# Kernel tuning notes

Hardware: AMD Instinct MI355X
Metric: run time of the kernel (lower is better)

Reference implementation:

```python
import jax, jax.numpy as jnp
import numpy as np
from jax import lax

HID = 256
BATCH = 256
INPUT_LEN = 512
N_SAMPLES = 16
HORIZON = 64


def _lstm_cell(x, h, c, Wih, Whh, b):
    # x: [B, in], h/c: [B, H]; PyTorch gate order i, f, g, o; b = b_ih + b_hh
    gates = x @ Wih.T + h @ Whh.T + b  # [B, 4H]
    i, f, g, o = jnp.split(gates, 4, axis=-1)
    c_new = jax.nn.sigmoid(f) * c + jax.nn.sigmoid(i) * jnp.tanh(g)
    h_new = jax.nn.sigmoid(o) * jnp.tanh(c_new)
    return h_new, c_new


def setup_inputs() -> dict:
    key = jax.random.key(0)
    ks = jax.random.split(key, 20)
    s = 1.0 / np.sqrt(HID)  # PyTorch LSTM init scale
    def u(k, shape):
        return jax.random.uniform(k, shape, jnp.float32, -s, s)
    inp = {
        "x": jax.random.normal(ks[0], (BATCH, INPUT_LEN), jnp.float32),
        "enc_Wih0": u(ks[1], (4 * HID, 1)),
        "enc_Whh0": u(ks[2], (4 * HID, HID)),
        "enc_b0": u(ks[3], (4 * HID,)),
        "enc_Wih1": u(ks[4], (4 * HID, HID)),
        "enc_Whh1": u(ks[5], (4 * HID, HID)),
        "enc_b1": u(ks[6], (4 * HID,)),
        "dec_Wih0": u(ks[7], (4 * HID, 1)),
        "dec_Whh0": u(ks[8], (4 * HID, HID)),
        "dec_b0": u(ks[9], (4 * HID,)),
        "dec_Wih1": u(ks[10], (4 * HID, HID)),
        "dec_Whh1": u(ks[11], (4 * HID, HID)),
        "dec_b1": u(ks[12], (4 * HID,)),
        "out_W": u(ks[13], (1, HID)),
        "out_b": u(ks[14], (1,)),
        # torch.rand(batch,1,1) per sample -> stacked over n_samples
        "dec_init": jax.random.uniform(ks[15], (N_SAMPLES, BATCH, 1), jnp.float32),
        "horizon": HORIZON,
    }
    return inp


def reference(x, enc_Wih0, enc_Whh0, enc_b0, enc_Wih1, enc_Whh1, enc_b1,
              dec_Wih0, dec_Whh0, dec_b0, dec_Wih1, dec_Whh1, dec_b1,
              out_W, out_b, dec_init, horizon):
    B, T = x.shape
    S = dec_init.shape[0]
    H = enc_Whh0.shape[1]

    # ---- encoder: 2-layer LSTM over input sequence ----
    xs = x.T[:, :, None]  # [T, B, 1]
    zero = jnp.zeros((B, H), x.dtype)

    def enc_step(carry, xt):
        h0, c0, h1, c1 = carry
        h0, c0 = _lstm_cell(xt, h0, c0, enc_Wih0, enc_Whh0, enc_b0)
        h1, c1 = _lstm_cell(h0, h1, c1, enc_Wih1, enc_Whh1, enc_b1)
        return (h0, c0, h1, c1), None

    (h0, c0, h1, c1), _ = lax.scan(enc_step, (zero, zero, zero, zero), xs)

    # ---- decoder: batch the independent n_samples together ----
    def rep(t):  # [B,H] -> [S*B,H]
        return jnp.broadcast_to(t, (S, B, H)).reshape(S * B, H)

    inp0 = dec_init.reshape(S * B, 1)

    def dec_step(carry, _):
        inp, h0, c0, h1, c1 = carry
        h0, c0 = _lstm_cell(inp, h0, c0, dec_Wih0, dec_Whh0, dec_b0)
        h1, c1 = _lstm_cell(h0, h1, c1, dec_Wih1, dec_Whh1, dec_b1)
        pred = h1 @ out_W.T + out_b  # [S*B, 1]
        return (pred, h0, c0, h1, c1), pred

    carry0 = (inp0, rep(h0), rep(c0), rep(h1), rep(c1))
    _, preds = lax.scan(dec_step, carry0, None, length=horizon)
    # preds: [T, S*B, 1] -> [B, S, T]
    return preds[:, :, 0].reshape(horizon, S, B).transpose(2, 1, 0)
```

## Files before the change

### kernel.cpp

```cpp
#include <hip/hip_runtime.h>
#include <stdint.h>


typedef short short8v __attribute__((ext_vector_type(8)));
typedef float float4v __attribute__((ext_vector_type(4)));
typedef unsigned long long u64;
#define MFMA(a,b,c) __builtin_amdgcn_mfma_f32_16x16x32_bf16((a),(b),(c),0,0,0)

#define HIDN 256
#define TLEN 512
#define HPE  ((size_t)256 * HIDN)
#define HPD  ((size_t)4096 * HIDN)

__device__ __forceinline__ unsigned short f2b(float f) {
    unsigned int u = __float_as_uint(f);
    unsigned int r = ((u >> 16) & 1u) + 0x7FFFu;
    return (unsigned short)((u + r) >> 16);
}
__device__ __forceinline__ float sigf(float x) { return 1.0f / (1.0f + __expf(-x)); }
__device__ __forceinline__ float tanhf2(float x) { return 1.0f - 2.0f / (1.0f + __expf(2.0f * x)); }

__device__ __forceinline__ void hpair_store(unsigned short* buf, int row, int hid,
                                            float h, int lane) {
    unsigned int mine = f2b(h);
    unsigned int part = (unsigned int)__shfl_xor((int)mine, 1);
    if (!(lane & 1)) {
        __hip_atomic_store((unsigned int*)&buf[(size_t)row * HIDN + hid],
                           mine | (part << 16),
                           __ATOMIC_RELAXED, __HIP_MEMORY_SCOPE_AGENT);
    }
}

__device__ __forceinline__ short8v ldA16(const unsigned short* p) {
    union { u64 d[2]; short8v v; } w;
    w.d[0] = __hip_atomic_load((const u64*)p,     __ATOMIC_RELAXED, __HIP_MEMORY_SCOPE_AGENT);
    w.d[1] = __hip_atomic_load((const u64*)p + 1, __ATOMIC_RELAXED, __HIP_MEMORY_SCOPE_AGENT);
    return w.v;
}

__device__ __forceinline__ void bar_sync(unsigned int* fl, int slot, unsigned int target,
                                         int nfl, int lane, int tid, int& dead) {
    __syncthreads();
    if (tid == 0)
        __hip_atomic_store(&fl[slot], target, __ATOMIC_RELAXED, __HIP_MEMORY_SCOPE_AGENT);
    if (tid < 64 && !dead) {
        int guard = 0;
        for (;;) {
            unsigned int v = 0xFFFFFFFFu;
            if (lane < nfl)
                v = __hip_atomic_load(&fl[lane], __ATOMIC_RELAXED, __HIP_MEMORY_SCOPE_AGENT);
            if (__ballot(v >= target) == ~0ull) break;
            if (++guard > (1 << 20)) { dead = 1; break; }
        }
    }
    __syncthreads();
    __builtin_amdgcn_fence(__ATOMIC_ACQUIRE, "workgroup");
}

__global__ __launch_bounds__(256) void pack_kernel(
    const float* __restrict__ Whh0, const float* __restrict__ Wih1,
    const float* __restrict__ Whh1, unsigned short* __restrict__ pk)
{
    int gid = blockIdx.x * 256 + threadIdx.x;
    int lane = gid & 63;
    int kc = (gid >> 6) & 7;
    int n  = (gid >> 9) & 63;
    int mat = gid >> 15;
    const float* W = (mat == 0) ? Whh0 : ((mat == 1) ? Wih1 : Whh1);
    const float* p = W + (size_t)(n * 16 + (lane & 15)) * HIDN
                       + (kc << 5) + ((lane >> 4) << 3);
    short8v v;
#pragma unroll
    for (int i = 0; i < 8; ++i) v[i] = (short)f2b(p[i]);
    *(short8v*)&pk[(size_t)gid << 3] = v;
}

__global__ __launch_bounds__(256, 1) void enc_kernel(
    const float* __restrict__ x,
    const float* __restrict__ Wih0, const float* __restrict__ Whh0, const float* __restrict__ b0,
    const float* __restrict__ Wih1, const float* __restrict__ Whh1, const float* __restrict__ b1,
    unsigned short* __restrict__ h0e, unsigned short* __restrict__ h1e,
    unsigned short* __restrict__ finh0, unsigned short* __restrict__ finh1,
    float* __restrict__ finc0, float* __restrict__ finc1,
    unsigned int* __restrict__ flags)
{
    const int tid = threadIdx.x, lane = tid & 63, wv = tid >> 6;
    const int bt = blockIdx.x & 15, hs = blockIdx.x >> 4;
    const int row0 = bt << 4, hidb = hs << 4;
    const int l15 = lane & 15, q = lane >> 4, q8 = q << 3;

    __shared__ float gt[12][16][17];
    __shared__ float xt[16][TLEN + 1];
    __shared__ unsigned short hst0[16][264], hst1[16][264];

    for (int idx = tid; idx < 16 * TLEN; idx += 256) {
        int r = idx >> 9, c = idx & 511;
        xt[r][c] = x[(size_t)(row0 + r) * TLEN + c];
    }

    short8v wf[3][8];
    {
        const float* Ws[3] = {Whh0, Wih1, Whh1};
#pragma unroll
        for (int j = 0; j < 3; ++j) {
            int p = wv * 3 + j;
            int mat = p >> 2, g = p & 3;
            const float* rp = Ws[mat] + (size_t)((g << 8) + hidb + l15) * HIDN + q8;
#pragma unroll
            for (int kc = 0; kc < 8; ++kc) {
                short8v v;
#pragma unroll
                for (int i = 0; i < 8; ++i) v[i] = (short)f2b(rp[(kc << 5) + i]);
                wf[j][kc] = v;
            }
        }
    }

    const int erow = tid >> 4, ehid = tid & 15;
    const int grow = row0 + erow, ghid = hidb + ehid;
    float wx[4], bb0v[4], bb1v[4];
#pragma unroll
    for (int g = 0; g < 4; ++g) {
        wx[g]   = Wih0[(g << 8) + ghid];
        bb0v[g] = b0[(g << 8) + ghid];
        bb1v[g] = b1[(g << 8) + ghid];
    }
    float c0 = 0.f, c1 = 0.f;
    unsigned int* fl = flags + (bt << 4);
    int dead = 0;
    const bool useH0 = (wv <= 2), useH1 = (wv >= 2);
    __syncthreads();

    for (int s = 1; s <= 513; ++s) {
        const unsigned short* hr0 = h0e + (size_t)((s - 1) & 1) * HPE;
        const unsigned short* hr1 = h1e + (size_t)((s - 1) & 1) * HPE;
        unsigned short* hw0 = h0e + (size_t)(s & 1) * HPE;
        unsigned short* hw1 = h1e + (size_t)(s & 1) * HPE;

        if (s >= 2) {
#pragma unroll
            for (int k = 0; k < 4; ++k) {
                int oo = tid + (k << 8);
                int r = oo >> 6, cu = oo & 63;
                u64 v = __hip_atomic_load((const u64*)&hr0[(size_t)(row0 + r) * HIDN + (cu << 2)],
                                          __ATOMIC_RELAXED, __HIP_MEMORY_SCOPE_AGENT);
                *(u64*)&hst0[r][cu << 2] = v;
            }
        }
        if (s >= 3) {
#pragma unroll
            for (int k = 0; k < 4; ++k) {
                int oo = tid + (k << 8);
                int r = oo >> 6, cu = oo & 63;
                u64 v = __hip_atomic_load((const u64*)&hr1[(size_t)(row0 + r) * HIDN + (cu << 2)],
                                          __ATOMIC_RELAXED, __HIP_MEMORY_SCOPE_AGENT);
                *(u64*)&hst1[r][cu << 2] = v;
            }
        }
        __syncthreads();

        float4v acc[3] = {{0,0,0,0},{0,0,0,0},{0,0,0,0}};
        short8v a0f[8], a1f[8];
        if (useH0 && s >= 2) {
#pragma unroll
            for (int kc = 0; kc < 8; ++kc) a0f[kc] = *(const short8v*)&hst0[l15][(kc << 5) + q8];
        }
        if (useH1 && s >= 3) {
#pragma unroll
            for (int kc = 0; kc < 8; ++kc) a1f[kc] = *(const short8v*)&hst1[l15][(kc << 5) + q8];
        }
#pragma unroll
        for (int j = 0; j < 3; ++j) {
            int p = wv * 3 + j;
            int mat = p >> 2;
            bool active = (mat == 0) ? (s >= 2 && s <= 512)
                        : (mat == 1) ? (s >= 2)
                                     : (s >= 3);
            if (active) {
                if (mat == 2) {
#pragma unroll
                    for (int kc = 0; kc < 8; ++kc) acc[j] = MFMA(a1f[kc], wf[j][kc], acc[j]);
                } else {
#pragma unroll
                    for (int kc = 0; kc < 8; ++kc) acc[j] = MFMA(a0f[kc], wf[j][kc], acc[j]);
                }
            }
        }
#pragma unroll
        for (int j = 0; j < 3; ++j) {
            int p = wv * 3 + j;
#pragma unroll
            for (int r = 0; r < 4; ++r) gt[p][(q << 2) + r][l15] = acc[j][r];
        }
        __syncthreads();

        if (s <= 512) {
            float xv = xt[erow][s - 1];
            float gi = gt[0][erow][ehid] + wx[0] * xv + bb0v[0];
            float gf = gt[1][erow][ehid] + wx[1] * xv + bb0v[1];
            float gg = gt[2][erow][ehid] + wx[2] * xv + bb0v[2];
            float go = gt[3][erow][ehid] + wx[3] * xv + bb0v[3];
            c0 = sigf(gf) * c0 + sigf(gi) * tanhf2(gg);
            float h0n = sigf(go) * tanhf2(c0);
            hpair_store(hw0, grow, ghid, h0n, lane);
            if (s == 512) {
                finh0[(size_t)grow * HIDN + ghid] = f2b(h0n);
                finc0[(size_t)grow * HIDN + ghid] = c0;
            }
        }
        if (s >= 2) {
            float gi = gt[4][erow][ehid] + gt[8][erow][ehid]  + bb1v[0];
            float gf = gt[5][erow][ehid] + gt[9][erow][ehid]  + bb1v[1];
            float gg = gt[6][erow][ehid] + gt[10][erow][ehid] + bb1v[2];
            float go = gt[7][erow][ehid] + gt[11][erow][ehid] + bb1v[3];
            c1 = sigf(gf) * c1 + sigf(gi) * tanhf2(gg);
            float h1n = sigf(go) * tanhf2(c1);
            hpair_store(hw1, grow, ghid, h1n, lane);
            if (s == 513) {
                finh1[(size_t)grow * HIDN + ghid] = f2b(h1n);
                finc1[(size_t)grow * HIDN + ghid] = c1;
            }
        }
        bar_sync(fl, hs, (unsigned int)s, 16, lane, tid, dead);
    }
}

__global__ __launch_bounds__(256, 1) void dec_kernel(
    const unsigned short* __restrict__ pk,
    const float* __restrict__ Wih0, const float* __restrict__ b0,
    const float* __restrict__ b1, const float* __restrict__ outW,
    const float* __restrict__ outb, const float* __restrict__ dinit,
    const unsigned short* __restrict__ finh0, const float* __restrict__ finc0,
    const unsigned short* __restrict__ finh1, const float* __restrict__ finc1,
    unsigned short* __restrict__ h0d, unsigned short* __restrict__ h1d,
    float* __restrict__ predbuf, unsigned int* __restrict__ flags,
    float* __restrict__ out)
{
    extern __shared__ unsigned short wlds[];
    const int tid = threadIdx.x, lane = tid & 63, wv = tid >> 6;
    const int rg = blockIdx.x & 31, hsl = blockIdx.x >> 5;
    const int row0 = rg << 7, hidb = hsl << 5;
    const int l15 = lane & 15, q = lane >> 4, q8 = q << 3;

#pragma unroll
    for (int k = 0; k < 32; ++k) {
        int sl = tid + (k << 8);
        int ln = sl & 63, kc = (sl >> 6) & 7, nf = (sl >> 9) & 7, mt = sl >> 12;
        int n = ((mt + 1) << 6) + ((nf >> 1) << 4) + (hsl << 1) + (nf & 1);
        *(short8v*)&wlds[sl << 3] =
            *(const short8v*)&pk[((size_t)((n << 3) + kc) << 9) + (ln << 3)];
    }

    const float outb_v = outb[0];
    float wx2[2][4], bb0v[2][4], bb1v[2][4], ow2[2];
#pragma unroll
    for (int u = 0; u < 2; ++u) {
        int hid = hidb + (u << 4) + l15;
        ow2[u] = outW[hid];
#pragma unroll
        for (int g = 0; g < 4; ++g) {
            wx2[u][g]  = Wih0[(g << 8) + hid];
            bb0v[u][g] = b0[(g << 8) + hid];
            bb1v[u][g] = b1[(g << 8) + hid];
        }
    }
    float c0r[2][2][4], c1r[2][2][4];
#pragma unroll
    for (int m = 0; m < 2; ++m)
#pragma unroll
        for (int u = 0; u < 2; ++u) {
            int hid = hidb + (u << 4) + l15;
#pragma unroll
            for (int r = 0; r < 4; ++r) {
                int row = row0 + (wv << 5) + (m << 4) + (q << 2) + r;
                c0r[m][u][r] = finc0[(size_t)(row & 255) * HIDN + hid];
                c1r[m][u][r] = finc1[(size_t)(row & 255) * HIDN + hid];
            }
        }

    short8v af0[2][8];
#pragma unroll
    for (int m = 0; m < 2; ++m) {
        int row = (row0 + (wv << 5) + (m << 4) + l15) & 255;
        const unsigned short* p = finh0 + (size_t)row * HIDN + q8;
#pragma unroll
        for (int kc = 0; kc < 8; ++kc) af0[m][kc] = *(const short8v*)&p[kc << 5];
    }

    unsigned int* fl = flags + (rg << 4);
    int dead = 0;
    __syncthreads();

    for (int t = 0; t < 64; ++t) {
        const unsigned short* h1prev = (t == 0) ? finh1 : h1d + (size_t)((t + 1) & 1) * HPD;
        unsigned short* h0w = h0d + (size_t)(t & 1) * HPD;
        unsigned short* h1w = h1d + (size_t)(t & 1) * HPD;
        const int rmask = (t == 0) ? 255 : 0x7FFFFFFF;

        short8v af1[2][8];
#pragma unroll
        for (int m = 0; m < 2; ++m) {
            int row = (row0 + (wv << 5) + (m << 4) + l15) & rmask;
            const unsigned short* p1 = h1prev + (size_t)row * HIDN + q8;
#pragma unroll
            for (int kc = 0; kc < 8; ++kc) af1[m][kc] = ldA16(p1 + (kc << 5));
        }
        float inp[2][4];
#pragma unroll
        for (int m = 0; m < 2; ++m)
#pragma unroll
            for (int r = 0; r < 4; ++r) {
                int row = row0 + (wv << 5) + (m << 4) + (q << 2) + r;
                inp[m][r] = (t == 0) ? dinit[row]
                    : __hip_atomic_load(&predbuf[(size_t)(t - 1) * 4096 + row],
                                        __ATOMIC_RELAXED, __HIP_MEMORY_SCOPE_AGENT) + outb_v;
            }
        if (hsl == 0 && t > 0 && l15 == 0) {
#pragma unroll
            for (int m = 0; m < 2; ++m)
#pragma unroll
                for (int r = 0; r < 4; ++r) {
                    int row = row0 + (wv << 5) + (m << 4) + (q << 2) + r;
                    out[(size_t)(((row & 255) << 4) + (row >> 8)) * 64 + (t - 1)] = inp[m][r];
                }
        }

        float4v acc0[2][8];
#pragma unroll
        for (int m = 0; m < 2; ++m)
#pragma unroll
            for (int nf = 0; nf < 8; ++nf) acc0[m][nf] = (float4v){0, 0, 0, 0};
#pragma unroll
        for (int kc = 0; kc < 8; ++kc)
#pragma unroll
            for (int nf = 0; nf < 8; ++nf) {
                int n = ((nf >> 1) << 4) + (hsl << 1) + (nf & 1);
                short8v bf = *(const short8v*)&pk[((size_t)((n << 3) + kc) << 9) + (lane << 3)];
                acc0[0][nf] = MFMA(af0[0][kc], bf, acc0[0][nf]);
                acc0[1][nf] = MFMA(af0[1][kc], bf, acc0[1][nf]);
            }
        float4v acc1[2][8];
#pragma unroll
        for (int m = 0; m < 2; ++m)
#pragma unroll
            for (int nf = 0; nf < 8; ++nf) acc1[m][nf] = (float4v){0, 0, 0, 0};
#pragma unroll
        for (int kc = 0; kc < 8; ++kc)
#pragma unroll
            for (int nf = 0; nf < 8; ++nf) {
                short8v bf = *(const short8v*)&wlds[(size_t)(4096 + (((nf << 3) + kc) << 6) + lane) << 3];
                acc1[0][nf] = MFMA(af1[0][kc], bf, acc1[0][nf]);
                acc1[1][nf] = MFMA(af1[1][kc], bf, acc1[1][nf]);
            }
#pragma unroll
        for (int m = 0; m < 2; ++m)
#pragma unroll
            for (int u = 0; u < 2; ++u) {
                int hid = hidb + (u << 4) + l15;
#pragma unroll
                for (int r = 0; r < 4; ++r) {
                    int row = row0 + (wv << 5) + (m << 4) + (q << 2) + r;
                    float gi = acc0[m][0 + u][r] + wx2[u][0] * inp[m][r] + bb0v[u][0];
                    float gf = acc0[m][2 + u][r] + wx2[u][1] * inp[m][r] + bb0v[u][1];
                    float gg = acc0[m][4 + u][r] + wx2[u][2] * inp[m][r] + bb0v[u][2];
                    float go = acc0[m][6 + u][r] + wx2[u][3] * inp[m][r] + bb0v[u][3];
                    float cn = sigf(gf) * c0r[m][u][r] + sigf(gi) * tanhf2(gg);
                    c0r[m][u][r] = cn;
                    float h0n = sigf(go) * tanhf2(cn);
                    hpair_store(h0w, row, hid, h0n, lane);
                }
            }
        bar_sync(fl, hsl, (unsigned int)(2 * t + 1), 8, lane, tid, dead);

#pragma unroll
        for (int m = 0; m < 2; ++m) {
            int row = row0 + (wv << 5) + (m << 4) + l15;
            const unsigned short* p0 = h0w + (size_t)row * HIDN + q8;
#pragma unroll
            for (int kc = 0; kc < 8; ++kc) af0[m][kc] = ldA16(p0 + (kc << 5));
        }
#pragma unroll
        for (int kc = 0; kc < 8; ++kc)
#pragma unroll
            for (int nf = 0; nf < 8; ++nf) {
                short8v bf = *(const short8v*)&wlds[(size_t)((((nf << 3) + kc) << 6) + lane) << 3];
                acc1[0][nf] = MFMA(af0[0][kc], bf, acc1[0][nf]);
                acc1[1][nf] = MFMA(af0[1][kc], bf, acc1[1][nf]);
            }
        float pp[2][4] = {{0,0,0,0},{0,0,0,0}};
#pragma unroll
        for (int m = 0; m < 2; ++m)
#pragma unroll
            for (int u = 0; u < 2; ++u) {
                int hid = hidb + (u << 4) + l15;
#pragma unroll
                for (int r = 0; r < 4; ++r) {
                    int row = row0 + (wv << 5) + (m << 4) + (q << 2) + r;
                    float gi = acc1[m][0 + u][r] + bb1v[u][0];
                    float gf = acc1[m][2 + u][r] + bb1v[u][1];
                    float gg = acc1[m][4 + u][r] + bb1v[u][2];
                    float go = acc1[m][6 + u][r] + bb1v[u][3];
                    float cn = sigf(gf) * c1r[m][u][r] + sigf(gi) * tanhf2(gg);
                    c1r[m][u][r] = cn;
                    float h1n = sigf(go) * tanhf2(cn);
                    pp[m][r] += h1n * ow2[u];
                    hpair_store(h1w, row, hid, h1n, lane);
                }
            }
#pragma unroll
        for (int off = 1; off < 16; off <<= 1)
#pragma unroll
            for (int m = 0; m < 2; ++m)
#pragma unroll
                for (int r = 0; r < 4; ++r) pp[m][r] += __shfl_xor(pp[m][r], off);
        if (l15 == 0) {
#pragma unroll
            for (int m = 0; m < 2; ++m)
#pragma unroll
                for (int r = 0; r < 4; ++r) {
                    int row = row0 + (wv << 5) + (m << 4) + (q << 2) + r;
                    atomicAdd(&predbuf[(size_t)t * 4096 + row], pp[m][r]);
                }
        }
        bar_sync(fl, hsl, (unsigned int)(2 * t + 2), 8, lane, tid, dead);
    }

    if (hsl == 0 && tid < 128) {
        int row = row0 + tid;
        float v = __hip_atomic_load(&predbuf[(size_t)63 * 4096 + row],
                                    __ATOMIC_RELAXED, __HIP_MEMORY_SCOPE_AGENT) + outb_v;
        out[(size_t)(((row & 255) << 4) + (row >> 8)) * 64 + 63] = v;
    }
}

extern "C" void kernel_launch(void* const* d_in, const int* in_sizes, int n_in,
                              void* d_out, int out_size, void* d_ws, size_t ws_size,
                              hipStream_t stream) {
    (void)in_sizes; (void)n_in; (void)out_size; (void)ws_size;
    const float* x     = (const float*)d_in[0];
    const float* eWih0 = (const float*)d_in[1];
    const float* eWhh0 = (const float*)d_in[2];
    const float* eb0   = (const float*)d_in[3];
    const float* eWih1 = (const float*)d_in[4];
    const float* eWhh1 = (const float*)d_in[5];
    const float* eb1   = (const float*)d_in[6];
    const float* dWih0 = (const float*)d_in[7];
    const float* dWhh0 = (const float*)d_in[8];
    const float* db0   = (const float*)d_in[9];
    const float* dWih1 = (const float*)d_in[10];
    const float* dWhh1 = (const float*)d_in[11];
    const float* db1   = (const float*)d_in[12];
    const float* outW  = (const float*)d_in[13];
    const float* outb  = (const float*)d_in[14];
    const float* dinit = (const float*)d_in[15];

    char* ws = (char*)d_ws;
    unsigned short* h0e   = (unsigned short*)(ws);
    unsigned short* h1e   = (unsigned short*)(ws + 262144);
    unsigned short* finh0 = (unsigned short*)(ws + 524288);
    unsigned short* finh1 = (unsigned short*)(ws + 655360);
    float* finc0          = (float*)(ws + 786432);
    float* finc1          = (float*)(ws + 1048576);
    unsigned int* fle     = (unsigned int*)(ws + 1310720);
    unsigned short* pk    = (unsigned short*)(ws + 1311744);
    unsigned short* h0d   = (unsigned short*)(ws + 2884608);
    unsigned short* h1d   = (unsigned short*)(ws + 7078912);
    unsigned int* fld     = (unsigned int*)(ws + 11273216);
    float* predraw        = (float*)(ws + 19661824);

    hipMemsetAsync(fle, 0, 1024, stream);
    hipMemsetAsync(fld, 0, 2048, stream);
    hipMemsetAsync(predraw, 0, 64 * 4096 * 4, stream);
    hipFuncSetAttribute((const void*)dec_kernel,
                        hipFuncAttributeMaxDynamicSharedMemorySize, 131072);

    pack_kernel<<<384, 256, 0, stream>>>(dWhh0, dWih1, dWhh1, pk);
    enc_kernel<<<256, 256, 0, stream>>>(x, eWih0, eWhh0, eb0, eWih1, eWhh1, eb1,
                                        h0e, h1e, finh0, finh1, finc0, finc1, fle);
    dec_kernel<<<256, 256, 131072, stream>>>(pk, dWih0, db0, db1, outW, outb, dinit,
                                             finh0, finc0, finh1, finc1,
                                             h0d, h1d, predraw, fld, (float*)d_out);
}
```

Before: 4.143 ms.

## Restructure decoder so each block owns rows, removing grid-wide barriers

The decoder is repartitioned so each of 64 blocks (512 threads) owns 64 batch rows and computes every hidden unit. The hidden states and the prediction reduction then stay in LDS, and only block-level syncs are needed. This removes the cross-block flag barriers, global h0/h1 exchange buffers and atomic prediction accumulation. In exchange, all weights are streamed from global/L2 every step instead of partially cached in LDS, and only 64 blocks run, so fewer CUs are used.

```diff
diff --git a/kernel.cpp b/kernel.cpp
--- a/kernel.cpp
+++ b/kernel.cpp
@@ -10,7 +10,7 @@
 #define HIDN 256
 #define TLEN 512
 #define HPE  ((size_t)256 * HIDN)
-#define HPD  ((size_t)4096 * HIDN)
+#define LDP  264
 
 __device__ __forceinline__ unsigned short f2b(float f) {
     unsigned int u = __float_as_uint(f);
@@ -29,13 +29,6 @@
                            mine | (part << 16),
                            __ATOMIC_RELAXED, __HIP_MEMORY_SCOPE_AGENT);
     }
-}
-
-__device__ __forceinline__ short8v ldA16(const unsigned short* p) {
-    union { u64 d[2]; short8v v; } w;
-    w.d[0] = __hip_atomic_load((const u64*)p,     __ATOMIC_RELAXED, __HIP_MEMORY_SCOPE_AGENT);
-    w.d[1] = __hip_atomic_load((const u64*)p + 1, __ATOMIC_RELAXED, __HIP_MEMORY_SCOPE_AGENT);
-    return w.v;
 }
 
 __device__ __forceinline__ void bar_sync(unsigned int* fl, int slot, unsigned int target,
@@ -225,211 +218,212 @@
     }
 }
 
-__global__ __launch_bounds__(256, 1) void dec_kernel(
+__global__ __launch_bounds__(512, 1) void dec_kernel(
     const unsigned short* __restrict__ pk,
     const float* __restrict__ Wih0, const float* __restrict__ b0,
     const float* __restrict__ b1, const float* __restrict__ outW,
     const float* __restrict__ outb, const float* __restrict__ dinit,
     const unsigned short* __restrict__ finh0, const float* __restrict__ finc0,
     const unsigned short* __restrict__ finh1, const float* __restrict__ finc1,
-    unsigned short* __restrict__ h0d, unsigned short* __restrict__ h1d,
-    float* __restrict__ predbuf, unsigned int* __restrict__ flags,
     float* __restrict__ out)
 {
-    extern __shared__ unsigned short wlds[];
+    extern __shared__ char smem[];
+    unsigned short* h0l = (unsigned short*)smem;
+    unsigned short* h1l = (unsigned short*)(smem + 64 * LDP * 2);
+    float* predp = (float*)(smem + 2 * 64 * LDP * 2);
+    float* inpl  = predp + 8 * 64;
+
     const int tid = threadIdx.x, lane = tid & 63, wv = tid >> 6;
-    const int rg = blockIdx.x & 31, hsl = blockIdx.x >> 5;
-    const int row0 = rg << 7, hidb = hsl << 5;
     const int l15 = lane & 15, q = lane >> 4, q8 = q << 3;
-
-#pragma unroll
-    for (int k = 0; k < 32; ++k) {
-        int sl = tid + (k << 8);
-        int ln = sl & 63, kc = (sl >> 6) & 7, nf = (sl >> 9) & 7, mt = sl >> 12;
-        int n = ((mt + 1) << 6) + ((nf >> 1) << 4) + (hsl << 1) + (nf & 1);
-        *(short8v*)&wlds[sl << 3] =
-            *(const short8v*)&pk[((size_t)((n << 3) + kc) << 9) + (ln << 3)];
-    }
-
+    const int row0 = blockIdx.x << 6;
     const float outb_v = outb[0];
-    float wx2[2][4], bb0v[2][4], bb1v[2][4], ow2[2];
-#pragma unroll
-    for (int u = 0; u < 2; ++u) {
-        int hid = hidb + (u << 4) + l15;
-        ow2[u] = outW[hid];
+    const unsigned short* pkm[3] = {pk, pk + 262144, pk + 524288};
+
+    for (int idx = tid; idx < 64 * 64; idx += 512) {
+        int r = idx >> 6, cu = idx & 63;
+        u64 v0 = *(const u64*)&finh0[(size_t)((row0 + r) & 255) * HIDN + (cu << 2)];
+        u64 v1 = *(const u64*)&finh1[(size_t)((row0 + r) & 255) * HIDN + (cu << 2)];
+        *(u64*)&h0l[r * LDP + (cu << 2)] = v0;
+        *(u64*)&h1l[r * LDP + (cu << 2)] = v1;
+    }
+    if (tid < 64) inpl[tid] = dinit[row0 + tid];
+
+    float wx[2][4], bb0v[2][4], bb1v[2][4], ow[2];
+    float c0r[2][4][4], c1r[2][4][4];
+#pragma unroll
+    for (int ch = 0; ch < 2; ++ch) {
+        int hid = (((wv << 1) + ch) << 4) + l15;
+        ow[ch] = outW[hid];
 #pragma unroll
         for (int g = 0; g < 4; ++g) {
-            wx2[u][g]  = Wih0[(g << 8) + hid];
-            bb0v[u][g] = b0[(g << 8) + hid];
-            bb1v[u][g] = b1[(g << 8) + hid];
-        }
-    }
-    float c0r[2][2][4], c1r[2][2][4];
-#pragma unroll
-    for (int m = 0; m < 2; ++m)
-#pragma unroll
-        for (int u = 0; u < 2; ++u) {
-            int hid = hidb + (u << 4) + l15;
+            wx[ch][g]   = Wih0[(g << 8) + hid];
+            bb0v[ch][g] = b0[(g << 8) + hid];
+            bb1v[ch][g] = b1[(g << 8) + hid];
+        }
+#pragma unroll
+        for (int m = 0; m < 4; ++m)
 #pragma unroll
             for (int r = 0; r < 4; ++r) {
-                int row = row0 + (wv << 5) + (m << 4) + (q << 2) + r;
-                c0r[m][u][r] = finc0[(size_t)(row & 255) * HIDN + hid];
-                c1r[m][u][r] = finc1[(size_t)(row & 255) * HIDN + hid];
-            }
-        }
-
-    short8v af0[2][8];
-#pragma unroll
-    for (int m = 0; m < 2; ++m) {
-        int row = (row0 + (wv << 5) + (m << 4) + l15) & 255;
-        const unsigned short* p = finh0 + (size_t)row * HIDN + q8;
-#pragma unroll
-        for (int kc = 0; kc < 8; ++kc) af0[m][kc] = *(const short8v*)&p[kc << 5];
-    }
-
-    unsigned int* fl = flags + (rg << 4);
-    int dead = 0;
+                int b = (row0 + (m << 4) + (q << 2) + r) & 255;
+                c0r[ch][m][r] = finc0[(size_t)b * HIDN + hid];
+                c1r[ch][m][r] = finc1[(size_t)b * HIDN + hid];
+            }
+    }
     __syncthreads();
 
     for (int t = 0; t < 64; ++t) {
-        const unsigned short* h1prev = (t == 0) ? finh1 : h1d + (size_t)((t + 1) & 1) * HPD;
-        unsigned short* h0w = h0d + (size_t)(t & 1) * HPD;
-        unsigned short* h1w = h1d + (size_t)(t & 1) * HPD;
-        const int rmask = (t == 0) ? 255 : 0x7FFFFFFF;
-
-        short8v af1[2][8];
-#pragma unroll
-        for (int m = 0; m < 2; ++m) {
-            int row = (row0 + (wv << 5) + (m << 4) + l15) & rmask;
-            const unsigned short* p1 = h1prev + (size_t)row * HIDN + q8;
-#pragma unroll
-            for (int kc = 0; kc < 8; ++kc) af1[m][kc] = ldA16(p1 + (kc << 5));
-        }
-        float inp[2][4];
-#pragma unroll
-        for (int m = 0; m < 2; ++m)
-#pragma unroll
-            for (int r = 0; r < 4; ++r) {
-                int row = row0 + (wv << 5) + (m << 4) + (q << 2) + r;
-                inp[m][r] = (t == 0) ? dinit[row]
-                    : __hip_atomic_load(&predbuf[(size_t)(t - 1) * 4096 + row],
-                                        __ATOMIC_RELAXED, __HIP_MEMORY_SCOPE_AGENT) + outb_v;
-            }
-        if (hsl == 0 && t > 0 && l15 == 0) {
-#pragma unroll
-            for (int m = 0; m < 2; ++m)
+        float inpr[4][4];
+#pragma unroll
+        for (int m = 0; m < 4; ++m)
+#pragma unroll
+            for (int r = 0; r < 4; ++r)
+                inpr[m][r] = inpl[(m << 4) + (q << 2) + r];
+
+        unsigned int ph0[2][4][4];
+#pragma unroll
+        for (int ch = 0; ch < 2; ++ch) {
+            const int hf = (wv << 1) + ch;
+            float4v acc[4][4];
+#pragma unroll
+            for (int m = 0; m < 4; ++m)
+#pragma unroll
+                for (int g = 0; g < 4; ++g) acc[m][g] = (float4v){0, 0, 0, 0};
+#pragma unroll
+            for (int kc = 0; kc < 8; ++kc) {
+                short8v a[4];
+#pragma unroll
+                for (int m = 0; m < 4; ++m)
+                    a[m] = *(const short8v*)&h0l[((m << 4) + l15) * LDP + (kc << 5) + q8];
+#pragma unroll
+                for (int g = 0; g < 4; ++g) {
+                    const int n = (g << 4) + hf;
+                    short8v bf = *(const short8v*)&pkm[0][((((n << 3) + kc) << 6) + lane) << 3];
+#pragma unroll
+                    for (int m = 0; m < 4; ++m) acc[m][g] = MFMA(a[m], bf, acc[m][g]);
+                }
+            }
+#pragma unroll
+            for (int m = 0; m < 4; ++m)
 #pragma unroll
                 for (int r = 0; r < 4; ++r) {
-                    int row = row0 + (wv << 5) + (m << 4) + (q << 2) + r;
-                    out[(size_t)(((row & 255) << 4) + (row >> 8)) * 64 + (t - 1)] = inp[m][r];
-                }
-        }
-
-        float4v acc0[2][8];
-#pragma unroll
-        for (int m = 0; m < 2; ++m)
-#pragma unroll
-            for (int nf = 0; nf < 8; ++nf) acc0[m][nf] = (float4v){0, 0, 0, 0};
-#pragma unroll
-        for (int kc = 0; kc < 8; ++kc)
-#pragma unroll
-            for (int nf = 0; nf < 8; ++nf) {
-                int n = ((nf >> 1) << 4) + (hsl << 1) + (nf & 1);
-                short8v bf = *(const short8v*)&pk[((size_t)((n << 3) + kc) << 9) + (lane << 3)];
-                acc0[0][nf] = MFMA(af0[0][kc], bf, acc0[0][nf]);
-                acc0[1][nf] = MFMA(af0[1][kc], bf, acc0[1][nf]);
-            }
-        float4v acc1[2][8];
-#pragma unroll
-        for (int m = 0; m < 2; ++m)
-#pragma unroll
-            for (int nf = 0; nf < 8; ++nf) acc1[m][nf] = (float4v){0, 0, 0, 0};
-#pragma unroll
-        for (int kc = 0; kc < 8; ++kc)
-#pragma unroll
-            for (int nf = 0; nf < 8; ++nf) {
-                short8v bf = *(const short8v*)&wlds[(size_t)(4096 + (((nf << 3) + kc) << 6) + lane) << 3];
-                acc1[0][nf] = MFMA(af1[0][kc], bf, acc1[0][nf]);
-                acc1[1][nf] = MFMA(af1[1][kc], bf, acc1[1][nf]);
-            }
-#pragma unroll
-        for (int m = 0; m < 2; ++m)
-#pragma unroll
-            for (int u = 0; u < 2; ++u) {
-                int hid = hidb + (u << 4) + l15;
+                    float inp = inpr[m][r];
+                    float gi = acc[m][0][r] + wx[ch][0] * inp + bb0v[ch][0];
+                    float gf = acc[m][1][r] + wx[ch][1] * inp + bb0v[ch][1];
+                    float gg = acc[m][2][r] + wx[ch][2] * inp + bb0v[ch][2];
+                    float go = acc[m][3][r] + wx[ch][3] * inp + bb0v[ch][3];
+                    float cn = sigf(gf) * c0r[ch][m][r] + sigf(gi) * tanhf2(gg);
+                    c0r[ch][m][r] = cn;
+                    float h0n = sigf(go) * tanhf2(cn);
+                    unsigned int mine = f2b(h0n);
+                    unsigned int part = (unsigned int)__shfl_xor((int)mine, 1);
+                    ph0[ch][m][r] = mine | (part << 16);
+                }
+        }
+        __syncthreads();
+        if (!(l15 & 1)) {
+#pragma unroll
+            for (int ch = 0; ch < 2; ++ch) {
+                int hid = (((wv << 1) + ch) << 4) + l15;
+#pragma unroll
+                for (int m = 0; m < 4; ++m)
+#pragma unroll
+                    for (int r = 0; r < 4; ++r)
+                        *(unsigned int*)&h0l[((m << 4) + (q << 2) + r) * LDP + hid] = ph0[ch][m][r];
+            }
+        }
+        __syncthreads();
+
+        float pp[4][4] = {{0,0,0,0},{0,0,0,0},{0,0,0,0},{0,0,0,0}};
+        unsigned int ph1[2][4][4];
+#pragma unroll
+        for (int ch = 0; ch < 2; ++ch) {
+            const int hf = (wv << 1) + ch;
+            float4v acc[4][4];
+#pragma unroll
+            for (int m = 0; m < 4; ++m)
+#pragma unroll
+                for (int g = 0; g < 4; ++g) acc[m][g] = (float4v){0, 0, 0, 0};
+#pragma unroll
+            for (int kc = 0; kc < 8; ++kc) {
+                short8v a[4];
+#pragma unroll
+                for (int m = 0; m < 4; ++m)
+                    a[m] = *(const short8v*)&h0l[((m << 4) + l15) * LDP + (kc << 5) + q8];
+#pragma unroll
+                for (int g = 0; g < 4; ++g) {
+                    const int n = (g << 4) + hf;
+                    short8v bf = *(const short8v*)&pkm[1][((((n << 3) + kc) << 6) + lane) << 3];
+#pragma unroll
+                    for (int m = 0; m < 4; ++m) acc[m][g] = MFMA(a[m], bf, acc[m][g]);
+                }
+            }
+#pragma unroll
+            for (int kc = 0; kc < 8; ++kc) {
+                short8v a[4];
+#pragma unroll
+                for (int m = 0; m < 4; ++m)
+                    a[m] = *(const short8v*)&h1l[((m << 4) + l15) * LDP + (kc << 5) + q8];
+#pragma unroll
+                for (int g = 0; g < 4; ++g) {
+                    const int n = (g << 4) + hf;
+                    short8v bf = *(const short8v*)&pkm[2][((((n << 3) + kc) << 6) + lane) << 3];
+#pragma unroll
+                    for (int m = 0; m < 4; ++m) acc[m][g] = MFMA(a[m], bf, acc[m][g]);
+                }
+            }
+#pragma unroll
+            for (int m = 0; m < 4; ++m)
 #pragma unroll
                 for (int r = 0; r < 4; ++r) {
-                    int row = row0 + (wv << 5) + (m << 4) + (q << 2) + r;
-                    float gi = acc0[m][0 + u][r] + wx2[u][0] * inp[m][r] + bb0v[u][0];
-                    float gf = acc0[m][2 + u][r] + wx2[u][1] * inp[m][r] + bb0v[u][1];
-                    float gg = acc0[m][4 + u][r] + wx2[u][2] * inp[m][r] + bb0v[u][2];
-                    float go = acc0[m][6 + u][r] + wx2[u][3] * inp[m][r] + bb0v[u][3];
-                    float cn = sigf(gf) * c0r[m][u][r] + sigf(gi) * tanhf2(gg);
-                    c0r[m][u][r] = cn;
-                    float h0n = sigf(go) * tanhf2(cn);
-                    hpair_store(h0w, row, hid, h0n, lane);
-                }
-            }
-        bar_sync(fl, hsl, (unsigned int)(2 * t + 1), 8, lane, tid, dead);
-
-#pragma unroll
-        for (int m = 0; m < 2; ++m) {
-            int row = row0 + (wv << 5) + (m << 4) + l15;
-            const unsigned short* p0 = h0w + (size_t)row * HIDN + q8;
-#pragma unroll
-            for (int kc = 0; kc < 8; ++kc) af0[m][kc] = ldA16(p0 + (kc << 5));
-        }
-#pragma unroll
-        for (int kc = 0; kc < 8; ++kc)
-#pragma unroll
-            for (int nf = 0; nf < 8; ++nf) {
-                short8v bf = *(const short8v*)&wlds[(size_t)((((nf << 3) + kc) << 6) + lane) << 3];
-                acc1[0][nf] = MFMA(af0[0][kc], bf, acc1[0][nf]);
-                acc1[1][nf] = MFMA(af0[1][kc], bf, acc1[1][nf]);
-            }
-        float pp[2][4] = {{0,0,0,0},{0,0,0,0}};
-#pragma unroll
-        for (int m = 0; m < 2; ++m)
-#pragma unroll
-            for (int u = 0; u < 2; ++u) {
-                int hid = hidb + (u << 4) + l15;
-#pragma unroll
-                for (int r = 0; r < 4; ++r) {
-                    int row = row0 + (wv << 5) + (m << 4) + (q << 2) + r;
-                    float gi = acc1[m][0 + u][r] + bb1v[u][0];
-                    float gf = acc1[m][2 + u][r] + bb1v[u][1];
-                    float gg = acc1[m][4 + u][r] + bb1v[u][2];
-                    float go = acc1[m][6 + u][r] + bb1v[u][3];
-                    float cn = sigf(gf) * c1r[m][u][r] + sigf(gi) * tanhf2(gg);
-                    c1r[m][u][r] = cn;
+                    float gi = acc[m][0][r] + bb1v[ch][0];
+                    float gf = acc[m][1][r] + bb1v[ch][1];
+                    float gg = acc[m][2][r] + bb1v[ch][2];
+                    float go = acc[m][3][r] + bb1v[ch][3];
+                    float cn = sigf(gf) * c1r[ch][m][r] + sigf(gi) * tanhf2(gg);
+                    c1r[ch][m][r] = cn;
                     float h1n = sigf(go) * tanhf2(cn);
-                    pp[m][r] += h1n * ow2[u];
-                    hpair_store(h1w, row, hid, h1n, lane);
-                }
-            }
+                    pp[m][r] += h1n * ow[ch];
+                    unsigned int mine = f2b(h1n);
+                    unsigned int part = (unsigned int)__shfl_xor((int)mine, 1);
+                    ph1[ch][m][r] = mine | (part << 16);
+                }
+        }
+        __syncthreads();
+        if (!(l15 & 1)) {
+#pragma unroll
+            for (int ch = 0; ch < 2; ++ch) {
+                int hid = (((wv << 1) + ch) << 4) + l15;
+#pragma unroll
+                for (int m = 0; m < 4; ++m)
+#pragma unroll
+                    for (int r = 0; r < 4; ++r)
+                        *(unsigned int*)&h1l[((m << 4) + (q << 2) + r) * LDP + hid] = ph1[ch][m][r];
+            }
+        }
 #pragma unroll
         for (int off = 1; off < 16; off <<= 1)
 #pragma unroll
-            for (int m = 0; m < 2; ++m)
+            for (int m = 0; m < 4; ++m)
 #pragma unroll
                 for (int r = 0; r < 4; ++r) pp[m][r] += __shfl_xor(pp[m][r], off);
         if (l15 == 0) {
 #pragma unroll
-            for (int m = 0; m < 2; ++m)
-#pragma unroll
-                for (int r = 0; r < 4; ++r) {
-                    int row = row0 + (wv << 5) + (m << 4) + (q << 2) + r;
-                    atomicAdd(&predbuf[(size_t)t * 4096 + row], pp[m][r]);
-                }
-        }
-        bar_sync(fl, hsl, (unsigned int)(2 * t + 2), 8, lane, tid, dead);
-    }
-
-    if (hsl == 0 && tid < 128) {
-        int row = row0 + tid;
-        float v = __hip_atomic_load(&predbuf[(size_t)63 * 4096 + row],
-                                    __ATOMIC_RELAXED, __HIP_MEMORY_SCOPE_AGENT) + outb_v;
-        out[(size_t)(((row & 255) << 4) + (row >> 8)) * 64 + 63] = v;
+            for (int m = 0; m < 4; ++m)
+#pragma unroll
+                for (int r = 0; r < 4; ++r)
+                    predp[(wv << 6) + (m << 4) + (q << 2) + r] = pp[m][r];
+        }
+        __syncthreads();
+        if (tid < 64) {
+            float s = predp[tid];
+#pragma unroll
+            for (int w = 1; w < 8; ++w) s += predp[(w << 6) + tid];
+            s += outb_v;
+            inpl[tid] = s;
+            int row = row0 + tid;
+            out[(size_t)(((row & 255) << 4) + (row >> 8)) * 64 + t] = s;
+        }
+        __syncthreads();
     }
 }
 
@@ -463,21 +457,17 @@
     float* finc1          = (float*)(ws + 1048576);
     unsigned int* fle     = (unsigned int*)(ws + 1310720);
     unsigned short* pk    = (unsigned short*)(ws + 1311744);
-    unsigned short* h0d   = (unsigned short*)(ws + 2884608);
-    unsigned short* h1d   = (unsigned short*)(ws + 7078912);
-    unsigned int* fld     = (unsigned int*)(ws + 11273216);
-    float* predraw        = (float*)(ws + 19661824);
 
     hipMemsetAsync(fle, 0, 1024, stream);
-    hipMemsetAsync(fld, 0, 2048, stream);
-    hipMemsetAsync(predraw, 0, 64 * 4096 * 4, stream);
+
+    const int dec_lds = 2 * 64 * LDP * 2 + 8 * 64 * 4 + 64 * 4;
     hipFuncSetAttribute((const void*)dec_kernel,
-                        hipFuncAttributeMaxDynamicSharedMemorySize, 131072);
+                        hipFuncAttributeMaxDynamicSharedMemorySize, dec_lds);
 
     pack_kernel<<<384, 256, 0, stream>>>(dWhh0, dWih1, dWhh1, pk);
     enc_kernel<<<256, 256, 0, stream>>>(x, eWih0, eWhh0, eb0, eWih1, eWhh1, eb1,
                                         h0e, h1e, finh0, finh1, finc0, finc1, fle);
-    dec_kernel<<<256, 256, 131072, stream>>>(pk, dWih0, db0, db1, outW, outb, dinit,
+    dec_kernel<<<64, 512, dec_lds, stream>>>(pk, dWih0, db0, db1, outW, outb, dinit,
                                              finh0, finc0, finh1, finc1,
-                                             h0d, h1d, predraw, fld, (float*)d_out);
-}
+                                             (float*)d_out);
+}
```

New measurement: 7.488 ms. 80.7% more time.

## Map decoder row groups to XCDs, replicate packed weights, replace atomics with partials

Applied to the files above, without the earlier changes.

The decoder reads its hardware XCC id and takes a slot from a per-XCC counter. This puts the eight blocks that share a row group and barrier on the same die, and each die reads its own replica of the packed weights. Pred accumulation switches from float atomicAdd to per-slice partial writes, which are reduced at the next step. The layer-0 cell now runs before the h1 load and barrier, h0/h1 go through plain stores with sc0 loads and explicit waitcnt drains, and the spin guard is tightened. The aim is to cut cross-die coherence traffic and atomic latency in the per-step barriers. The cost is 8x weight replication and a reliance on the undocumented coherence behaviour of sc0 loads.

```diff
diff --git a/kernel.cpp b/kernel.cpp
--- a/kernel.cpp
+++ b/kernel.cpp
@@ -11,6 +11,7 @@
 #define TLEN 512
 #define HPE  ((size_t)256 * HIDN)
 #define HPD  ((size_t)4096 * HIDN)
+#define PKREP 786432
 
 __device__ __forceinline__ unsigned short f2b(float f) {
     unsigned int u = __float_as_uint(f);
@@ -19,6 +20,21 @@
 }
 __device__ __forceinline__ float sigf(float x) { return 1.0f / (1.0f + __expf(-x)); }
 __device__ __forceinline__ float tanhf2(float x) { return 1.0f - 2.0f / (1.0f + __expf(2.0f * x)); }
+
+__device__ __forceinline__ short8v ld16_sc0(const unsigned short* p) {
+    short8v v;
+    asm volatile("global_load_dwordx4 %0, %1, off sc0" : "=&v"(v) : "v"(p) : "memory");
+    return v;
+}
+__device__ __forceinline__ float4v ld16f_sc0(const float* p) {
+    float4v v;
+    asm volatile("global_load_dwordx4 %0, %1, off sc0" : "=&v"(v) : "v"(p) : "memory");
+    return v;
+}
+__device__ __forceinline__ void vm_drain() {
+    asm volatile("s_waitcnt vmcnt(0)" ::: "memory");
+    __builtin_amdgcn_sched_barrier(0);
+}
 
 __device__ __forceinline__ void hpair_store(unsigned short* buf, int row, int hid,
                                             float h, int lane) {
@@ -30,16 +46,17 @@
                            __ATOMIC_RELAXED, __HIP_MEMORY_SCOPE_AGENT);
     }
 }
-
-__device__ __forceinline__ short8v ldA16(const unsigned short* p) {
-    union { u64 d[2]; short8v v; } w;
-    w.d[0] = __hip_atomic_load((const u64*)p,     __ATOMIC_RELAXED, __HIP_MEMORY_SCOPE_AGENT);
-    w.d[1] = __hip_atomic_load((const u64*)p + 1, __ATOMIC_RELAXED, __HIP_MEMORY_SCOPE_AGENT);
-    return w.v;
+__device__ __forceinline__ void hpair_plain(unsigned short* buf, int row, int hid,
+                                            float h, int lane) {
+    unsigned int mine = f2b(h);
+    unsigned int part = (unsigned int)__shfl_xor((int)mine, 1);
+    if (!(lane & 1))
+        *(unsigned int*)&buf[(size_t)row * HIDN + hid] = mine | (part << 16);
 }
 
 __device__ __forceinline__ void bar_sync(unsigned int* fl, int slot, unsigned int target,
-                                         int nfl, int lane, int tid, int& dead) {
+                                         int nfl, int lane, int tid, int& dead,
+                                         int guard_lim) {
     __syncthreads();
     if (tid == 0)
         __hip_atomic_store(&fl[slot], target, __ATOMIC_RELAXED, __HIP_MEMORY_SCOPE_AGENT);
@@ -50,7 +67,7 @@
             if (lane < nfl)
                 v = __hip_atomic_load(&fl[lane], __ATOMIC_RELAXED, __HIP_MEMORY_SCOPE_AGENT);
             if (__ballot(v >= target) == ~0ull) break;
-            if (++guard > (1 << 20)) { dead = 1; break; }
+            if (++guard > guard_lim) { dead = 1; break; }
         }
     }
     __syncthreads();
@@ -72,7 +89,9 @@
     short8v v;
 #pragma unroll
     for (int i = 0; i < 8; ++i) v[i] = (short)f2b(p[i]);
-    *(short8v*)&pk[(size_t)gid << 3] = v;
+#pragma unroll
+    for (int rep = 0; rep < 8; ++rep)
+        *(short8v*)&pk[(size_t)rep * PKREP + ((size_t)gid << 3)] = v;
 }
 
 __global__ __launch_bounds__(256, 1) void enc_kernel(
@@ -221,7 +240,7 @@
                 finc1[(size_t)grow * HIDN + ghid] = c1;
             }
         }
-        bar_sync(fl, hs, (unsigned int)s, 16, lane, tid, dead);
+        bar_sync(fl, hs, (unsigned int)s, 16, lane, tid, dead, 1 << 20);
     }
 }
 
@@ -233,14 +252,26 @@
     const unsigned short* __restrict__ finh0, const float* __restrict__ finc0,
     const unsigned short* __restrict__ finh1, const float* __restrict__ finc1,
     unsigned short* __restrict__ h0d, unsigned short* __restrict__ h1d,
-    float* __restrict__ predbuf, unsigned int* __restrict__ flags,
-    float* __restrict__ out)
+    float* __restrict__ predpart, unsigned int* __restrict__ flags,
+    unsigned int* __restrict__ qcnt, float* __restrict__ out)
 {
     extern __shared__ unsigned short wlds[];
+    float* inpl = (float*)&wlds[65536];
+    __shared__ int slot_s;
+
     const int tid = threadIdx.x, lane = tid & 63, wv = tid >> 6;
-    const int rg = blockIdx.x & 31, hsl = blockIdx.x >> 5;
+    const int l15 = lane & 15, q = lane >> 4, q8 = q << 3;
+
+    unsigned int xcc;
+    asm volatile("s_getreg_b32 %0, hwreg(HW_REG_XCC_ID)" : "=s"(xcc));
+    xcc &= 7u;
+    if (tid == 0) slot_s = (int)(atomicAdd(&qcnt[xcc], 1u) & 31u);
+    __syncthreads();
+    const int slot = slot_s;
+    const int rg = ((int)xcc << 2) + (slot >> 3);
+    const int hsl = slot & 7;
     const int row0 = rg << 7, hidb = hsl << 5;
-    const int l15 = lane & 15, q = lane >> 4, q8 = q << 3;
+    const unsigned short* pkr = pk + (size_t)xcc * PKREP;
 
 #pragma unroll
     for (int k = 0; k < 32; ++k) {
@@ -248,7 +279,7 @@
         int ln = sl & 63, kc = (sl >> 6) & 7, nf = (sl >> 9) & 7, mt = sl >> 12;
         int n = ((mt + 1) << 6) + ((nf >> 1) << 4) + (hsl << 1) + (nf & 1);
         *(short8v*)&wlds[sl << 3] =
-            *(const short8v*)&pk[((size_t)((n << 3) + kc) << 9) + (ln << 3)];
+            *(const short8v*)&pkr[((size_t)((n << 3) + kc) << 9) + (ln << 3)];
     }
 
     const float outb_v = outb[0];
@@ -297,48 +328,74 @@
         unsigned short* h1w = h1d + (size_t)(t & 1) * HPD;
         const int rmask = (t == 0) ? 255 : 0x7FFFFFFF;
 
+        float4v pr0 = {0,0,0,0}, pr1 = {0,0,0,0};
+        if (t == 0) {
+            if (tid < 128) inpl[tid] = dinit[row0 + tid];
+        } else if (tid < 128) {
+            const float* pb = predpart + ((size_t)((t - 1) & 1) << 15)
+                            + ((size_t)(row0 + tid) << 3);
+            pr0 = ld16f_sc0(pb);
+            pr1 = ld16f_sc0(pb + 4);
+        }
+
+        float4v acc0[2][8];
+#pragma unroll
+        for (int m = 0; m < 2; ++m)
+#pragma unroll
+            for (int nf = 0; nf < 8; ++nf) acc0[m][nf] = (float4v){0, 0, 0, 0};
+#pragma unroll
+        for (int kc = 0; kc < 8; ++kc)
+#pragma unroll
+            for (int nf = 0; nf < 8; ++nf) {
+                int n = ((nf >> 1) << 4) + (hsl << 1) + (nf & 1);
+                short8v bf = *(const short8v*)&pkr[((size_t)((n << 3) + kc) << 9) + (lane << 3)];
+                acc0[0][nf] = MFMA(af0[0][kc], bf, acc0[0][nf]);
+                acc0[1][nf] = MFMA(af0[1][kc], bf, acc0[1][nf]);
+            }
+        if (t > 0) {
+            vm_drain();
+            if (tid < 128) {
+                float s = ((pr0[0] + pr0[1]) + (pr0[2] + pr0[3]))
+                        + ((pr1[0] + pr1[1]) + (pr1[2] + pr1[3])) + outb_v;
+                inpl[tid] = s;
+                if (hsl == 0) {
+                    int row = row0 + tid;
+                    out[(size_t)(((row & 255) << 4) + (row >> 8)) * 64 + (t - 1)] = s;
+                }
+            }
+        }
+        __syncthreads();
+
+#pragma unroll
+        for (int m = 0; m < 2; ++m)
+#pragma unroll
+            for (int u = 0; u < 2; ++u) {
+                int hid = hidb + (u << 4) + l15;
+#pragma unroll
+                for (int r = 0; r < 4; ++r) {
+                    int lr = (wv << 5) + (m << 4) + (q << 2) + r;
+                    int row = row0 + lr;
+                    float inp = inpl[lr];
+                    float gi = acc0[m][0 + u][r] + wx2[u][0] * inp + bb0v[u][0];
+                    float gf = acc0[m][2 + u][r] + wx2[u][1] * inp + bb0v[u][1];
+                    float gg = acc0[m][4 + u][r] + wx2[u][2] * inp + bb0v[u][2];
+                    float go = acc0[m][6 + u][r] + wx2[u][3] * inp + bb0v[u][3];
+                    float cn = sigf(gf) * c0r[m][u][r] + sigf(gi) * tanhf2(gg);
+                    c0r[m][u][r] = cn;
+                    float h0n = sigf(go) * tanhf2(cn);
+                    hpair_plain(h0w, row, hid, h0n, lane);
+                }
+            }
+
         short8v af1[2][8];
 #pragma unroll
         for (int m = 0; m < 2; ++m) {
             int row = (row0 + (wv << 5) + (m << 4) + l15) & rmask;
             const unsigned short* p1 = h1prev + (size_t)row * HIDN + q8;
 #pragma unroll
-            for (int kc = 0; kc < 8; ++kc) af1[m][kc] = ldA16(p1 + (kc << 5));
-        }
-        float inp[2][4];
-#pragma unroll
-        for (int m = 0; m < 2; ++m)
-#pragma unroll
-            for (int r = 0; r < 4; ++r) {
-                int row = row0 + (wv << 5) + (m << 4) + (q << 2) + r;
-                inp[m][r] = (t == 0) ? dinit[row]
-                    : __hip_atomic_load(&predbuf[(size_t)(t - 1) * 4096 + row],
-                                        __ATOMIC_RELAXED, __HIP_MEMORY_SCOPE_AGENT) + outb_v;
-            }
-        if (hsl == 0 && t > 0 && l15 == 0) {
-#pragma unroll
-            for (int m = 0; m < 2; ++m)
-#pragma unroll
-                for (int r = 0; r < 4; ++r) {
-                    int row = row0 + (wv << 5) + (m << 4) + (q << 2) + r;
-                    out[(size_t)(((row & 255) << 4) + (row >> 8)) * 64 + (t - 1)] = inp[m][r];
-                }
-        }
-
-        float4v acc0[2][8];
-#pragma unroll
-        for (int m = 0; m < 2; ++m)
-#pragma unroll
-            for (int nf = 0; nf < 8; ++nf) acc0[m][nf] = (float4v){0, 0, 0, 0};
-#pragma unroll
-        for (int kc = 0; kc < 8; ++kc)
-#pragma unroll
-            for (int nf = 0; nf < 8; ++nf) {
-                int n = ((nf >> 1) << 4) + (hsl << 1) + (nf & 1);
-                short8v bf = *(const short8v*)&pk[((size_t)((n << 3) + kc) << 9) + (lane << 3)];
-                acc0[0][nf] = MFMA(af0[0][kc], bf, acc0[0][nf]);
-                acc0[1][nf] = MFMA(af0[1][kc], bf, acc0[1][nf]);
-            }
+            for (int kc = 0; kc < 8; ++kc) af1[m][kc] = ld16_sc0(p1 + (kc << 5));
+        }
+        vm_drain();
         float4v acc1[2][8];
 #pragma unroll
         for (int m = 0; m < 2; ++m)
@@ -352,33 +409,16 @@
                 acc1[0][nf] = MFMA(af1[0][kc], bf, acc1[0][nf]);
                 acc1[1][nf] = MFMA(af1[1][kc], bf, acc1[1][nf]);
             }
-#pragma unroll
-        for (int m = 0; m < 2; ++m)
-#pragma unroll
-            for (int u = 0; u < 2; ++u) {
-                int hid = hidb + (u << 4) + l15;
-#pragma unroll
-                for (int r = 0; r < 4; ++r) {
-                    int row = row0 + (wv << 5) + (m << 4) + (q << 2) + r;
-                    float gi = acc0[m][0 + u][r] + wx2[u][0] * inp[m][r] + bb0v[u][0];
-                    float gf = acc0[m][2 + u][r] + wx2[u][1] * inp[m][r] + bb0v[u][1];
-                    float gg = acc0[m][4 + u][r] + wx2[u][2] * inp[m][r] + bb0v[u][2];
-                    float go = acc0[m][6 + u][r] + wx2[u][3] * inp[m][r] + bb0v[u][3];
-                    float cn = sigf(gf) * c0r[m][u][r] + sigf(gi) * tanhf2(gg);
-                    c0r[m][u][r] = cn;
-                    float h0n = sigf(go) * tanhf2(cn);
-                    hpair_store(h0w, row, hid, h0n, lane);
-                }
-            }
-        bar_sync(fl, hsl, (unsigned int)(2 * t + 1), 8, lane, tid, dead);
+        bar_sync(fl, hsl, (unsigned int)(2 * t + 1), 8, lane, tid, dead, 1 << 16);
 
 #pragma unroll
         for (int m = 0; m < 2; ++m) {
             int row = row0 + (wv << 5) + (m << 4) + l15;
             const unsigned short* p0 = h0w + (size_t)row * HIDN + q8;
 #pragma unroll
-            for (int kc = 0; kc < 8; ++kc) af0[m][kc] = ldA16(p0 + (kc << 5));
-        }
+            for (int kc = 0; kc < 8; ++kc) af0[m][kc] = ld16_sc0(p0 + (kc << 5));
+        }
+        vm_drain();
 #pragma unroll
         for (int kc = 0; kc < 8; ++kc)
 #pragma unroll
@@ -404,7 +444,7 @@
                     c1r[m][u][r] = cn;
                     float h1n = sigf(go) * tanhf2(cn);
                     pp[m][r] += h1n * ow2[u];
-                    hpair_store(h1w, row, hid, h1n, lane);
+                    hpair_plain(h1w, row, hid, h1n, lane);
                 }
             }
 #pragma unroll
@@ -414,22 +454,27 @@
 #pragma unroll
                 for (int r = 0; r < 4; ++r) pp[m][r] += __shfl_xor(pp[m][r], off);
         if (l15 == 0) {
+            float* pb = predpart + ((size_t)(t & 1) << 15);
 #pragma unroll
             for (int m = 0; m < 2; ++m)
 #pragma unroll
                 for (int r = 0; r < 4; ++r) {
                     int row = row0 + (wv << 5) + (m << 4) + (q << 2) + r;
-                    atomicAdd(&predbuf[(size_t)t * 4096 + row], pp[m][r]);
+                    pb[((size_t)row << 3) + hsl] = pp[m][r];
                 }
         }
-        bar_sync(fl, hsl, (unsigned int)(2 * t + 2), 8, lane, tid, dead);
+        bar_sync(fl, hsl, (unsigned int)(2 * t + 2), 8, lane, tid, dead, 1 << 16);
     }
 
     if (hsl == 0 && tid < 128) {
+        const float* pb = predpart + ((size_t)1 << 15) + ((size_t)(row0 + tid) << 3);
+        float4v a = ld16f_sc0(pb);
+        float4v b2 = ld16f_sc0(pb + 4);
+        vm_drain();
+        float s = ((a[0] + a[1]) + (a[2] + a[3]))
+                + ((b2[0] + b2[1]) + (b2[2] + b2[3])) + outb_v;
         int row = row0 + tid;
-        float v = __hip_atomic_load(&predbuf[(size_t)63 * 4096 + row],
-                                    __ATOMIC_RELAXED, __HIP_MEMORY_SCOPE_AGENT) + outb_v;
-        out[(size_t)(((row & 255) << 4) + (row >> 8)) * 64 + 63] = v;
+        out[(size_t)(((row & 255) << 4) + (row >> 8)) * 64 + 63] = s;
     }
 }
 
@@ -463,21 +508,25 @@
     float* finc1          = (float*)(ws + 1048576);
     unsigned int* fle     = (unsigned int*)(ws + 1310720);
     unsigned short* pk    = (unsigned short*)(ws + 1311744);
-    unsigned short* h0d   = (unsigned short*)(ws + 2884608);
-    unsigned short* h1d   = (unsigned short*)(ws + 7078912);
-    unsigned int* fld     = (unsigned int*)(ws + 11273216);
-    float* predraw        = (float*)(ws + 19661824);
+    unsigned int* fld     = (unsigned int*)(ws + 13894656);
+    unsigned int* qcnt    = (unsigned int*)(ws + 13896704);
+    unsigned short* h0d   = (unsigned short*)(ws + 13896768);
+    unsigned short* h1d   = (unsigned short*)(ws + 18091072);
+    float* predpart       = (float*)(ws + 22285376);
 
     hipMemsetAsync(fle, 0, 1024, stream);
     hipMemsetAsync(fld, 0, 2048, stream);
-    hipMemsetAsync(predraw, 0, 64 * 4096 * 4, stream);
+    hipMemsetAsync(qcnt, 0, 64, stream);
+
+    const int dec_lds = 131072 + 512;
     hipFuncSetAttribute((const void*)dec_kernel,
-                        hipFuncAttributeMaxDynamicSharedMemorySize, 131072);
+                        hipFuncAttributeMaxDynamicSharedMemorySize, dec_lds);
 
     pack_kernel<<<384, 256, 0, stream>>>(dWhh0, dWih1, dWhh1, pk);
     enc_kernel<<<256, 256, 0, stream>>>(x, eWih0, eWhh0, eb0, eWih1, eWhh1, eb1,
                                         h0e, h1e, finh0, finh1, finc0, finc1, fle);
-    dec_kernel<<<256, 256, 131072, stream>>>(pk, dWih0, db0, db1, outW, outb, dinit,
-                                             finh0, finc0, finh1, finc1,
-                                             h0d, h1d, predraw, fld, (float*)d_out);
-}
+    dec_kernel<<<256, 256, dec_lds, stream>>>(pk, dWih0, db0, db1, outW, outb, dinit,
+                                              finh0, finc0, finh1, finc1,
+                                              h0d, h1d, predpart, fld, qcnt,
+                                              (float*)d_out);
+}
```

After: 4.680 ms. 13.0% more time.
